# Optimization experiments

Hardware: AMD Instinct MI355X
Metric: run time of the kernel (lower is better)

The kernel has to match this reference:

```python
import jax, jax.numpy as jnp
import numpy as np
from jax import lax

KH, KW, PAD = 3, 3, 1  # kernel_size and paddings from init_kwargs


def _sign_pm1(v):
    # tf.sign with zeros mapped to -1
    return jnp.where(v > 0, jnp.float32(1.0), jnp.float32(-1.0)).astype(v.dtype)


def setup_inputs() -> dict:
    key = jax.random.key(0)
    k1, k2, k3 = jax.random.split(key, 3)
    x = jax.random.normal(k1, (32, 56, 56, 256), dtype=jnp.float32)
    kernel = jax.random.normal(k2, (KH, KW, 256, 256), dtype=jnp.float32) * 0.05
    bias = jax.random.normal(k3, (256,), dtype=jnp.float32) * 0.01
    return {"x": x, "kernel": kernel, "bias": bias}


def reference(x, kernel, bias):
    # pad input spatially (NHWC)
    xp = jnp.pad(x, ((0, 0), (PAD, PAD), (PAD, PAD), (0, 0)))

    # binarize kernel: static batch dim known -> alpha = mean(|W|) over (kh, kw, cin)
    bin_k = _sign_pm1(kernel)
    alpha = jnp.mean(jnp.abs(kernel), axis=(0, 1, 2))  # (Cout,)

    # binarize input: batch dim dynamic in TF -> beta = mean(|x|) over channels, keepdims
    bin_x = _sign_pm1(xp)                               # (N, H+2P, W+2P, C)
    beta = jnp.mean(jnp.abs(xp), axis=3, keepdims=True)  # (N, H+2P, W+2P, 1)

    # K = avg_pool(beta, kernel window, stride 1, VALID)
    K = lax.reduce_window(beta, jnp.float32(0.0), lax.add,
                          (1, KH, KW, 1), (1, 1, 1, 1), 'VALID') / (KH * KW)
    Ka = K * alpha  # (N, H, W, Cout) via broadcast

    conv = lax.conv_general_dilated(
        bin_x, bin_k, window_strides=(1, 1), padding='VALID',
        dimension_numbers=('NHWC', 'HWIO', 'NHWC'))  # (N, H, W, Cout)

    return conv * Ka + bias
```

## Files before the change

kernel.cpp:

```cpp
#include <hip/hip_runtime.h>
#include <cstdint>

#define N_ 32
#define H_ 56
#define W_ 56
#define C_ 256
#define HP 58
#define WP 58


__global__ __launch_bounds__(256) void pack_w(const float* __restrict__ k,
                                              uint64_t* __restrict__ kb,
                                              float* __restrict__ palpha) {
    int idx = blockIdx.x;
    int p = idx >> 2, j = idx & 3;
    int co = threadIdx.x;
    uint64_t bits = 0;
    float s = 0.f;
    #pragma unroll
    for (int b = 0; b < 64; ++b) {
        float v = k[(p * 256 + 4 * b + j) * 256 + co];
        bits |= (uint64_t)(v > 0.f) << b;
        s += fabsf(v);
    }
    kb[((size_t)p * 256 + co) * 4 + j] = bits;
    palpha[idx * 256 + co] = s;
}

__global__ __launch_bounds__(256) void pack_x(const float4* __restrict__ x4,
                                              uint64_t* __restrict__ xb,
                                              float* __restrict__ beta) {
    int bi = blockIdx.x;
    int n = bi / HP, y = bi % HP;
    int wave = threadIdx.x >> 6, lane = threadIdx.x & 63;
    for (int xc = wave; xc < WP; xc += 4) {
        bool inb = (y >= 1 && y <= H_ && xc >= 1 && xc <= W_);
        float4 v = make_float4(0.f, 0.f, 0.f, 0.f);
        if (inb)
            v = x4[(((size_t)n * H_ + (y - 1)) * W_ + (xc - 1)) * 64 + lane];
        uint64_t m0 = __ballot(v.x > 0.f);
        uint64_t m1 = __ballot(v.y > 0.f);
        uint64_t m2 = __ballot(v.z > 0.f);
        uint64_t m3 = __ballot(v.w > 0.f);
        float s = fabsf(v.x) + fabsf(v.y) + fabsf(v.z) + fabsf(v.w);
        #pragma unroll
        for (int m = 32; m >= 1; m >>= 1) s += __shfl_xor(s, m, 64);
        size_t pix = (size_t)bi * WP + xc;
        if (lane < 4) {
            uint64_t mw = (lane == 0) ? m0 : (lane == 1) ? m1 : (lane == 2) ? m2 : m3;
            xb[pix * 4 + lane] = mw;
        }
        if (lane == 0) beta[pix] = s * (1.f / 256.f);
    }
}

__global__ __launch_bounds__(256, 4) void bconv(
        const uint64_t* __restrict__ xb, const float* __restrict__ beta,
        const uint64_t* __restrict__ kb, const float* __restrict__ palpha,
        const float* __restrict__ bias, float* __restrict__ out) {
    int bi = blockIdx.x;
    int n = bi / H_, h = bi % H_;
    int tid = threadIdx.x;
    int half = tid >> 7;
    int col = tid & 127;
    int co = (blockIdx.y << 7) | col;

    __shared__ __align__(16) uint64_t xs[3 * WP * 4];
    __shared__ float brow[3 * WP];
    __shared__ float bS[W_];
    __shared__ uint32_t pb[128 * 15];

    const uint64_t* xsrc = xb + (size_t)(n * HP + h) * WP * 4;
    for (int i = tid; i < 3 * WP * 2; i += 256)
        ((ulonglong2*)xs)[i] = ((const ulonglong2*)xsrc)[i];
    const float* bsrc = beta + (size_t)(n * HP + h) * WP;
    for (int i = tid; i < 3 * WP; i += 256) brow[i] = bsrc[i];
    __syncthreads();

    if (tid < W_) {
        float s = 0.f;
        #pragma unroll
        for (int r = 0; r < 3; ++r)
            #pragma unroll
            for (int d = 0; d < 3; ++d) s += brow[r * WP + tid + d];
        bS[tid] = s * (1.f / 9.f);
    }

    uint64_t kr0[9], kr1[9];
    #pragma unroll
    for (int t = 0; t < 9; ++t) {
        ulonglong2 kp = ((const ulonglong2*)kb)[((size_t)t * 256 + co) * 2 + half];
        kr0[t] = kp.x;
        kr1[t] = kp.y;
    }
    float asum = 0.f;
    #pragma unroll
    for (int i = 0; i < 36; ++i) asum += palpha[i * 256 + co];
    float alpha = asum * (1.f / 2304.f);
    float bv = bias[co];

    for (int chunk = 0; chunk < 4; ++chunk) {
        int w0 = chunk * 14;
        uint32_t acc[14];
        #pragma unroll
        for (int i = 0; i < 14; ++i) acc[i] = 0;

        const uint64_t* base = &xs[w0 * 4 + 2 * half];
        #pragma unroll
        for (int xi = 0; xi < 16; ++xi) {
            #pragma unroll
            for (int r = 0; r < 3; ++r) {
                uint64_t x0 = base[(r * WP + xi) * 4];
                uint64_t x1 = base[(r * WP + xi) * 4 + 1];
                #pragma unroll
                for (int kw = 0; kw < 3; ++kw) {
                    int wl = xi - kw;
                    if (wl >= 0 && wl < 14) {
                        int t = r * 3 + kw;
                        acc[wl] += __popcll(x0 ^ kr0[t]) + __popcll(x1 ^ kr1[t]);
                    }
                }
            }
        }

        __syncthreads();
        if (half == 1) {
            #pragma unroll
            for (int i = 0; i < 14; ++i) pb[col * 15 + i] = acc[i];
        }
        __syncthreads();
        if (half == 0) {
            #pragma unroll
            for (int i = 0; i < 14; ++i) {
                int w = w0 + i;
                int tot = (int)(acc[i] + pb[col * 15 + i]);
                float conv = (float)(2304 - 2 * tot);
                out[((size_t)bi * W_ + w) * C_ + co] = conv * bS[w] * alpha + bv;
            }
        }
    }
}

extern "C" void kernel_launch(void* const* d_in, const int* in_sizes, int n_in,
                              void* d_out, int out_size, void* d_ws, size_t ws_size,
                              hipStream_t stream) {
    const float* x    = (const float*)d_in[0];
    const float* k    = (const float*)d_in[1];
    const float* bias = (const float*)d_in[2];
    float* out = (float*)d_out;

    char* ws = (char*)d_ws;
    uint64_t* kb     = (uint64_t*)(ws);
    float*    palpha = (float*)(ws + 73728);
    uint64_t* xb     = (uint64_t*)(ws + 110592);
    float*    beta   = (float*)(ws + 3555328);

    pack_w<<<36, 256, 0, stream>>>(k, kb, palpha);
    pack_x<<<N_ * HP, 256, 0, stream>>>((const float4*)x, xb, beta);
    bconv<<<dim3(N_ * H_, 2), 256, 0, stream>>>(xb, beta, kb, palpha, bias, out);
}
```

Measured before the change: 294.0 us.

## Replace XOR-popcount binary conv with int8 MFMA implicit GEMM

Binarized activations and weights are now stored as ±1 int8 values instead of packed bits, and the convolution runs as an implicit GEMM using 32x32x32 int8 MFMA instructions. Each block covers two output rows and all 256 output channels, staging a swizzled 4-row input tile in LDS, and blocks are remapped across the grid. This moves the work off scalar popcount ALU onto matrix cores. The cost is an activation buffer eight times larger to write and read, plus a much larger shared-memory footprint per block.

Result: no change. 293.3 us (-0.3%).

```diff
diff --git a/kernel.cpp b/kernel.cpp
--- a/kernel.cpp
+++ b/kernel.cpp
@@ -1,5 +1,6 @@
 #include <hip/hip_runtime.h>
 #include <cstdint>
+#include <cstddef>
 
 #define N_ 32
 #define H_ 56
@@ -8,27 +9,42 @@
 #define HP 58
 #define WP 58
 
+typedef int v4i  __attribute__((ext_vector_type(4)));
+typedef int v16i __attribute__((ext_vector_type(16)));
 
 __global__ __launch_bounds__(256) void pack_w(const float* __restrict__ k,
-                                              uint64_t* __restrict__ kb,
+                                              signed char* __restrict__ wi8,
                                               float* __restrict__ palpha) {
     int idx = blockIdx.x;
-    int p = idx >> 2, j = idx & 3;
+    int p = idx >> 2, q = idx & 3;
     int co = threadIdx.x;
-    uint64_t bits = 0;
     float s = 0.f;
     #pragma unroll
-    for (int b = 0; b < 64; ++b) {
-        float v = k[(p * 256 + 4 * b + j) * 256 + co];
-        bits |= (uint64_t)(v > 0.f) << b;
-        s += fabsf(v);
-    }
-    kb[((size_t)p * 256 + co) * 4 + j] = bits;
+    for (int half = 0; half < 2; ++half) {
+        int kc = q * 2 + half;
+        unsigned wrd[8];
+        #pragma unroll
+        for (int e = 0; e < 8; ++e) {
+            unsigned wv = 0;
+            #pragma unroll
+            for (int j = 0; j < 4; ++j) {
+                float v = k[(size_t)(p * 256 + kc * 32 + e * 4 + j) * 256 + co];
+                s += fabsf(v);
+                wv |= ((v > 0.f) ? 0x01u : 0xFFu) << (8 * j);
+            }
+            wrd[e] = wv;
+        }
+        v4i lo = {(int)wrd[0], (int)wrd[1], (int)wrd[2], (int)wrd[3]};
+        v4i hi = {(int)wrd[4], (int)wrd[5], (int)wrd[6], (int)wrd[7]};
+        size_t base = ((size_t)(p * 8 + kc) * 256 + co) * 2;
+        ((v4i*)wi8)[base]     = lo;
+        ((v4i*)wi8)[base + 1] = hi;
+    }
     palpha[idx * 256 + co] = s;
 }
 
 __global__ __launch_bounds__(256) void pack_x(const float4* __restrict__ x4,
-                                              uint64_t* __restrict__ xb,
+                                              signed char* __restrict__ xi8,
                                               float* __restrict__ beta) {
     int bi = blockIdx.x;
     int n = bi / HP, y = bi % HP;
@@ -38,107 +54,132 @@
         float4 v = make_float4(0.f, 0.f, 0.f, 0.f);
         if (inb)
             v = x4[(((size_t)n * H_ + (y - 1)) * W_ + (xc - 1)) * 64 + lane];
-        uint64_t m0 = __ballot(v.x > 0.f);
-        uint64_t m1 = __ballot(v.y > 0.f);
-        uint64_t m2 = __ballot(v.z > 0.f);
-        uint64_t m3 = __ballot(v.w > 0.f);
+        unsigned w = ((v.x > 0.f) ? 0x01u : 0xFFu)
+                   | (((v.y > 0.f) ? 0x01u : 0xFFu) << 8)
+                   | (((v.z > 0.f) ? 0x01u : 0xFFu) << 16)
+                   | (((v.w > 0.f) ? 0x01u : 0xFFu) << 24);
         float s = fabsf(v.x) + fabsf(v.y) + fabsf(v.z) + fabsf(v.w);
         #pragma unroll
         for (int m = 32; m >= 1; m >>= 1) s += __shfl_xor(s, m, 64);
         size_t pix = (size_t)bi * WP + xc;
-        if (lane < 4) {
-            uint64_t mw = (lane == 0) ? m0 : (lane == 1) ? m1 : (lane == 2) ? m2 : m3;
-            xb[pix * 4 + lane] = mw;
-        }
+        ((unsigned*)xi8)[pix * 64 + lane] = w;
         if (lane == 0) beta[pix] = s * (1.f / 256.f);
     }
 }
 
-__global__ __launch_bounds__(256, 4) void bconv(
-        const uint64_t* __restrict__ xb, const float* __restrict__ beta,
-        const uint64_t* __restrict__ kb, const float* __restrict__ palpha,
+__device__ __forceinline__ void epilogue(const v16i& acc, int mb, int svar,
+                                         const float* bS, float alpha, float bv,
+                                         int co, size_t obase,
+                                         float* __restrict__ out) {
+    #pragma unroll
+    for (int r = 0; r < 16; ++r) {
+        int row = (r & 3) + 8 * (r >> 2) + 4 * svar;
+        int m = mb + row;
+        if (m < 112) {
+            int hl = (m >= 56);
+            int w = m - 56 * hl;
+            float val = (float)acc[r] * (bS[m] * alpha) + bv;
+            out[obase + ((size_t)hl * W_ + w) * C_ + co] = val;
+        }
+    }
+}
+
+__global__ __launch_bounds__(512, 4) void bconv(
+        const signed char* __restrict__ xi8, const float* __restrict__ beta,
+        const signed char* __restrict__ wi8, const float* __restrict__ palpha,
         const float* __restrict__ bias, float* __restrict__ out) {
-    int bi = blockIdx.x;
-    int n = bi / H_, h = bi % H_;
+    int bid = blockIdx.x;
+    int bi = (bid & 7) * 112 + (bid >> 3);
+    int n = bi / 28;
+    int hb = (bi - n * 28) * 2;
+
     int tid = threadIdx.x;
-    int half = tid >> 7;
-    int col = tid & 127;
-    int co = (blockIdx.y << 7) | col;
-
-    __shared__ __align__(16) uint64_t xs[3 * WP * 4];
-    __shared__ float brow[3 * WP];
-    __shared__ float bS[W_];
-    __shared__ uint32_t pb[128 * 15];
-
-    const uint64_t* xsrc = xb + (size_t)(n * HP + h) * WP * 4;
-    for (int i = tid; i < 3 * WP * 2; i += 256)
-        ((ulonglong2*)xs)[i] = ((const ulonglong2*)xsrc)[i];
-    const float* bsrc = beta + (size_t)(n * HP + h) * WP;
-    for (int i = tid; i < 3 * WP; i += 256) brow[i] = bsrc[i];
+    int lane = tid & 63, wid = tid >> 6;
+    int wm = wid >> 2, wn = wid & 3;
+    int l31 = lane & 31, svar = lane >> 5;
+
+    __shared__ __align__(16) signed char xs[4 * WP * 256];
+    __shared__ float brow[4 * WP];
+    __shared__ float bS[112];
+
+    {
+        const v4i* src = (const v4i*)(xi8 + (size_t)(n * HP + hb) * WP * 256);
+        v4i* dst = (v4i*)xs;
+        for (int s = tid; s < 4 * WP * 16; s += 512) {
+            int pp = s >> 4, sl = s & 15;
+            dst[(pp << 4) | (sl ^ (pp & 15))] = src[s];
+        }
+        const float* bsrc = beta + (size_t)(n * HP + hb) * WP;
+        for (int i = tid; i < 4 * WP; i += 512) brow[i] = bsrc[i];
+    }
     __syncthreads();
 
-    if (tid < W_) {
+    if (tid < 112) {
+        int r = (tid >= 56);
+        int w = tid - 56 * r;
         float s = 0.f;
         #pragma unroll
-        for (int r = 0; r < 3; ++r)
+        for (int rr = 0; rr < 3; ++rr)
             #pragma unroll
-            for (int d = 0; d < 3; ++d) s += brow[r * WP + tid + d];
+            for (int d = 0; d < 3; ++d) s += brow[(r + rr) * WP + w + d];
         bS[tid] = s * (1.f / 9.f);
     }
 
-    uint64_t kr0[9], kr1[9];
-    #pragma unroll
-    for (int t = 0; t < 9; ++t) {
-        ulonglong2 kp = ((const ulonglong2*)kb)[((size_t)t * 256 + co) * 2 + half];
-        kr0[t] = kp.x;
-        kr1[t] = kp.y;
-    }
-    float asum = 0.f;
-    #pragma unroll
-    for (int i = 0; i < 36; ++i) asum += palpha[i * 256 + co];
-    float alpha = asum * (1.f / 2304.f);
-    float bv = bias[co];
-
-    for (int chunk = 0; chunk < 4; ++chunk) {
-        int w0 = chunk * 14;
-        uint32_t acc[14];
-        #pragma unroll
-        for (int i = 0; i < 14; ++i) acc[i] = 0;
-
-        const uint64_t* base = &xs[w0 * 4 + 2 * half];
-        #pragma unroll
-        for (int xi = 0; xi < 16; ++xi) {
-            #pragma unroll
-            for (int r = 0; r < 3; ++r) {
-                uint64_t x0 = base[(r * WP + xi) * 4];
-                uint64_t x1 = base[(r * WP + xi) * 4 + 1];
-                #pragma unroll
-                for (int kw = 0; kw < 3; ++kw) {
-                    int wl = xi - kw;
-                    if (wl >= 0 && wl < 14) {
-                        int t = r * 3 + kw;
-                        acc[wl] += __popcll(x0 ^ kr0[t]) + __popcll(x1 ^ kr1[t]);
-                    }
-                }
-            }
-        }
-
-        __syncthreads();
-        if (half == 1) {
-            #pragma unroll
-            for (int i = 0; i < 14; ++i) pb[col * 15 + i] = acc[i];
-        }
-        __syncthreads();
-        if (half == 0) {
-            #pragma unroll
-            for (int i = 0; i < 14; ++i) {
-                int w = w0 + i;
-                int tot = (int)(acc[i] + pb[col * 15 + i]);
-                float conv = (float)(2304 - 2 * tot);
-                out[((size_t)bi * W_ + w) * C_ + co] = conv * bS[w] * alpha + bv;
-            }
-        }
-    }
+    int m0 = wm * 64 + l31;
+    int m1 = m0 + 32;
+    int m1e = m1 < 112 ? m1 : 111;
+    int hl0 = (m0 >= 56), hl1 = (m1e >= 56);
+    int pb0 = hl0 * WP + (m0 - 56 * hl0);
+    int pb1 = hl1 * WP + (m1e - 56 * hl1);
+
+    int co0 = wn * 64 + l31, co1 = co0 + 32;
+    int vb0 = co0 * 2 + svar, vb1 = vb0 + 64;
+
+    v16i acc00 = {0,0,0,0,0,0,0,0,0,0,0,0,0,0,0,0};
+    v16i acc01 = acc00, acc10 = acc00, acc11 = acc00;
+
+    const v4i* xsv = (const v4i*)xs;
+    const v4i* wv  = (const v4i*)wi8;
+
+    for (int tap = 0; tap < 9; ++tap) {
+        int kh = (tap * 11) >> 5;
+        int kw = tap - kh * 3;
+        int p0 = pb0 + kh * WP + kw;
+        int p1 = pb1 + kh * WP + kw;
+        int a0 = p0 << 4, x0 = p0 & 15;
+        int a1 = p1 << 4, x1 = p1 & 15;
+        const v4i* bq = wv + (size_t)tap * 8 * 512;
+        #pragma unroll
+        for (int kc = 0; kc < 8; ++kc) {
+            int sl = kc * 2 + svar;
+            v4i A0 = xsv[a0 | (sl ^ x0)];
+            v4i A1 = xsv[a1 | (sl ^ x1)];
+            v4i B0 = bq[vb0];
+            v4i B1 = bq[vb1];
+            acc00 = __builtin_amdgcn_mfma_i32_32x32x32_i8(A0, B0, acc00, 0, 0, 0);
+            acc01 = __builtin_amdgcn_mfma_i32_32x32x32_i8(A0, B1, acc01, 0, 0, 0);
+            acc10 = __builtin_amdgcn_mfma_i32_32x32x32_i8(A1, B0, acc10, 0, 0, 0);
+            acc11 = __builtin_amdgcn_mfma_i32_32x32x32_i8(A1, B1, acc11, 0, 0, 0);
+            bq += 512;
+        }
+    }
+
+    __syncthreads();
+
+    float a0s = 0.f, a1s = 0.f;
+    for (int i = 0; i < 36; ++i) {
+        a0s += palpha[i * 256 + co0];
+        a1s += palpha[i * 256 + co1];
+    }
+    a0s *= (1.f / 2304.f);
+    a1s *= (1.f / 2304.f);
+    float bv0 = bias[co0], bv1 = bias[co1];
+
+    size_t obase = (size_t)(n * H_ + hb) * W_ * C_;
+    epilogue(acc00, wm * 64,      svar, bS, a0s, bv0, co0, obase, out);
+    epilogue(acc01, wm * 64,      svar, bS, a1s, bv1, co1, obase, out);
+    epilogue(acc10, wm * 64 + 32, svar, bS, a0s, bv0, co0, obase, out);
+    epilogue(acc11, wm * 64 + 32, svar, bS, a1s, bv1, co1, obase, out);
 }
 
 extern "C" void kernel_launch(void* const* d_in, const int* in_sizes, int n_in,
@@ -150,12 +191,12 @@
     float* out = (float*)d_out;
 
     char* ws = (char*)d_ws;
-    uint64_t* kb     = (uint64_t*)(ws);
-    float*    palpha = (float*)(ws + 73728);
-    uint64_t* xb     = (uint64_t*)(ws + 110592);
-    float*    beta   = (float*)(ws + 3555328);
-
-    pack_w<<<36, 256, 0, stream>>>(k, kb, palpha);
-    pack_x<<<N_ * HP, 256, 0, stream>>>((const float4*)x, xb, beta);
-    bconv<<<dim3(N_ * H_, 2), 256, 0, stream>>>(xb, beta, kb, palpha, bias, out);
-}
+    signed char* wi8    = (signed char*)(ws);
+    float*       palpha = (float*)(ws + 589824);
+    signed char* xi8    = (signed char*)(ws + 626688);
+    float*       beta   = (float*)(ws + 28184576);
+
+    pack_w<<<36, 256, 0, stream>>>(k, wi8, palpha);
+    pack_x<<<N_ * HP, 256, 0, stream>>>((const float4*)x, xi8, beta);
+    bconv<<<896, 512, 0, stream>>>(xi8, beta, wi8, palpha, bias, out);
+}
```
